# Kernel optimization log

Measured on AMD Instinct MI355X. Metric: run time of the kernel, lower is better.

Reference implementation:

```python
import jax, jax.numpy as jnp
import numpy as np

B, S, E, H = 1, 2048, 1024, 16
D = E // H          # head_dim = 64
SM_SCALE = 0.5      # module default, not 1/sqrt(D)


def setup_inputs() -> dict:
    key = jax.random.key(0)
    ks = jax.random.split(key, 9)
    std = 0.02
    return {
        "x":  jax.random.normal(ks[0], (B, S, E), dtype=jnp.float32),
        "Wq": jax.random.normal(ks[1], (E, E), dtype=jnp.float32) * std,
        "bq": jnp.zeros((E,), dtype=jnp.float32),
        "Wk": jax.random.normal(ks[2], (E, E), dtype=jnp.float32) * std,
        "bk": jnp.zeros((E,), dtype=jnp.float32),
        "Wv": jax.random.normal(ks[3], (E, E), dtype=jnp.float32) * std,
        "bv": jnp.zeros((E,), dtype=jnp.float32),
        "Wo": jax.random.normal(ks[4], (E, E), dtype=jnp.float32) * std,
        "bo": jnp.zeros((E,), dtype=jnp.float32),
    }


def _split_heads(t):
    # [B,S,E] -> [B,H,S,D]
    b, s, _ = t.shape
    return jnp.transpose(t.reshape(b, s, H, D), (0, 2, 1, 3))


def reference(x, Wq, bq, Wk, bk, Wv, bv, Wo, bo):
    # Projections in fp32, then cast to bf16 (matches module's .astype(bf16))
    q = _split_heads((x @ Wq + bq).astype(jnp.bfloat16))
    k = _split_heads((x @ Wk + bk).astype(jnp.bfloat16))
    v = _split_heads((x @ Wv + bv).astype(jnp.bfloat16))

    # Blockwise loop in the original is mathematically full causal attention
    scores = jnp.einsum("bhqd,bhkd->bhqk", q, k) * SM_SCALE  # [B,H,S,S] bf16
    causal = jnp.tril(jnp.ones((S, S), dtype=bool))
    scores = jnp.where(causal[None, None, :, :], scores, -jnp.inf)
    probs = jax.nn.softmax(scores, axis=-1)
    out = jnp.einsum("bhqk,bhkd->bhqd", probs, v)            # [B,H,S,D]

    out = jnp.transpose(out, (0, 2, 1, 3)).reshape(B, S, E)
    # dropout off (is_training=False / rate=0); final projection in fp32
    return out.astype(jnp.float32) @ Wo + bo
```

## Files before the change

### kernel.cpp

```cpp
#include <hip/hip_runtime.h>
#include <hip/hip_bf16.h>

#define S_LEN 2048
#define E_DIM 1024
#define NH    16
#define HD    64
#define SM_SCALE 0.5f

typedef short bf16x8_t __attribute__((ext_vector_type(8)));
typedef float f32x4_t  __attribute__((ext_vector_type(4)));
typedef __bf16 bf16x4_t __attribute__((ext_vector_type(4)));

static __device__ __forceinline__ unsigned short f2bf_bits(float f) {
    return __builtin_bit_cast(unsigned short, (__bf16)f);
}

#define GLD16(gp, lp) __builtin_amdgcn_global_load_lds(                       \
    (const __attribute__((address_space(1))) void*)(gp),                      \
    (__attribute__((address_space(3))) void*)(lp), 16, 0, 0)

__global__ void k_prep(const float* __restrict__ x,
                       const float* __restrict__ Wq, const float* __restrict__ Wk,
                       const float* __restrict__ Wv, const float* __restrict__ Wo,
                       __bf16* __restrict__ xb, __bf16* __restrict__ wt) {
    const int z = blockIdx.z;
    if (z < 4) {
        __shared__ float tile[32][33];
        const float* W = z == 0 ? Wq : z == 1 ? Wk : z == 2 ? Wv : Wo;
        __bf16* o = wt + (size_t)z * E_DIM * E_DIM;
        const int tx = threadIdx.x, ty = threadIdx.y;
        const int bx = blockIdx.x * 32, by = blockIdx.y * 32;
#pragma unroll
        for (int j = 0; j < 32; j += 8)
            tile[ty + j][tx] = W[(size_t)(by + ty + j) * E_DIM + bx + tx];
        __syncthreads();
#pragma unroll
        for (int j = 0; j < 32; j += 8)
            o[(size_t)(bx + ty + j) * E_DIM + by + tx] = (__bf16)tile[tx][ty + j];
    } else {
        const int bid = (z - 4) * 1024 + blockIdx.y * 32 + blockIdx.x;
        const int tid = threadIdx.y * 32 + threadIdx.x;
        const int i = bid * 256 + tid;
        const float4 v = ((const float4*)x)[i];
        bf16x4_t o4;
        o4.x = (__bf16)v.x; o4.y = (__bf16)v.y; o4.z = (__bf16)v.z; o4.w = (__bf16)v.w;
        ((bf16x4_t*)xb)[i] = o4;
    }
}

__global__ __launch_bounds__(256) void k_gemm_qkv(
    const __bf16* __restrict__ xb, const __bf16* __restrict__ wt,
    const float* __restrict__ bq, const float* __restrict__ bk, const float* __restrict__ bv,
    __bf16* __restrict__ qkv) {
    __shared__ __align__(16) unsigned short As[128 * 32];
    __shared__ __align__(16) unsigned short Bs[128 * 32];

    const int z = blockIdx.z;
    const __bf16* Bt = wt + (size_t)z * E_DIM * E_DIM;
    const float* bias = z == 0 ? bq : z == 1 ? bk : bv;
    __bf16* out = qkv + (size_t)z * NH * S_LEN * HD;

    const int tid = threadIdx.x, w = tid >> 6, l = tid & 63;
    const int lm = l & 15, q4 = l >> 4;
    const int bm = blockIdx.y, bn = blockIdx.x;
    const int wm = w >> 1, wn = w & 1;

    const int sm = (w << 4) + (l >> 2);
    const int skk = (l & 3) << 3;
    const __bf16* Ag = xb + (size_t)(bm * 128 + sm) * E_DIM + skk;
    const __bf16* Bg = Bt + (size_t)(bn * 128 + sm) * E_DIM + skk;
    unsigned short* AsW = As + (w << 9);
    unsigned short* BsW = Bs + (w << 9);

    f32x4_t acc[4][4];
#pragma unroll
    for (int i = 0; i < 4; i++)
#pragma unroll
        for (int j = 0; j < 4; j++) { acc[i][j].x = 0.f; acc[i][j].y = 0.f; acc[i][j].z = 0.f; acc[i][j].w = 0.f; }

    for (int k0 = 0; k0 < E_DIM; k0 += 32) {
        __syncthreads();
        GLD16(Ag + k0, AsW);
        GLD16(Ag + (size_t)64 * E_DIM + k0, AsW + 2048);
        GLD16(Bg + k0, BsW);
        GLD16(Bg + (size_t)64 * E_DIM + k0, BsW + 2048);
        __syncthreads();

        bf16x8_t af[4], bfr[4];
#pragma unroll
        for (int mt = 0; mt < 4; mt++)
            af[mt] = *(const bf16x8_t*)&As[(wm * 64 + mt * 16 + lm) * 32 + q4 * 8];
#pragma unroll
        for (int nt = 0; nt < 4; nt++)
            bfr[nt] = *(const bf16x8_t*)&Bs[(wn * 64 + nt * 16 + lm) * 32 + q4 * 8];
#pragma unroll
        for (int mt = 0; mt < 4; mt++)
#pragma unroll
            for (int nt = 0; nt < 4; nt++)
                acc[mt][nt] = __builtin_amdgcn_mfma_f32_16x16x32_bf16(af[mt], bfr[nt], acc[mt][nt], 0, 0, 0);
    }

#pragma unroll
    for (int nt = 0; nt < 4; nt++) {
        const int n = bn * 128 + wn * 64 + nt * 16 + lm;
        const float bval = bias[n];
        const int h = n >> 6, d = n & 63;
        const int tile0 = bm * 2 + wm;
        if (z == 2) {
            const int t4 = d >> 4, flm = d & 15;
#pragma unroll
            for (int mt = 0; mt < 4; mt++) {
                const int q4p = (mt * 2 + (q4 >> 1)) & 3;
                const int j0 = (q4 & 1) * 4;
                __bf16* ob = out + ((((size_t)h * 32 + tile0) * 4 + t4) * 2 + (mt >> 1)) * 512
                                 + (q4p * 16 + flm) * 8 + j0;
                union { unsigned short s[4]; uint2 u; } pk;
#pragma unroll
                for (int i = 0; i < 4; i++) pk.s[i] = f2bf_bits(acc[mt][nt][i] + bval);
                *(uint2*)ob = pk.u;
            }
        } else {
            const float scale = (z == 0) ? SM_SCALE : 1.0f;
            const int c = d >> 5, q4p = (d >> 3) & 3, j = d & 7;
#pragma unroll
            for (int mt = 0; mt < 4; mt++) {
                __bf16* ob = out + ((((size_t)h * 32 + tile0) * 4 + mt) * 2 + c) * 512
                                 + (q4p * 16 + q4 * 4) * 8 + j;
#pragma unroll
                for (int i = 0; i < 4; i++)
                    ob[i * 8] = (__bf16)((acc[mt][nt][i] + bval) * scale);
            }
        }
    }
}

__global__ __launch_bounds__(256, 2) void k_attn(
    const __bf16* __restrict__ Qf, const __bf16* __restrict__ Kf, const __bf16* __restrict__ Vf,
    __bf16* __restrict__ attn) {
    __shared__ __align__(16) unsigned short KVs[2][2][4096];
    __shared__ __align__(16) unsigned short Pl[4][16 * 72];

    const int b = blockIdx.x;
    int qt, h;
    if (b < 256) { qt = 16 + (b >> 4); h = b & 15; }
    else         { qt = 15 - ((b - 256) >> 4); h = (b - 256) & 15; }

    const int tid = threadIdx.x, w = tid >> 6, l = tid & 63;
    const int lm = l & 15, q4 = l >> 4;

    const __bf16* Qb = Qf + ((size_t)h * 32 + qt) * 4096;
    const __bf16* Kb = Kf + (size_t)h * 32 * 4096;
    const __bf16* Vb = Vf + (size_t)h * 32 * 4096;

    bf16x8_t qf[2];
#pragma unroll
    for (int c = 0; c < 2; c++)
        qf[c] = *(const bf16x8_t*)(Qb + ((w * 2 + c) << 9) + l * 8);

    float lacc = 0.f;
    f32x4_t oacc[4];
#pragma unroll
    for (int t = 0; t < 4; t++) { oacc[t].x = 0.f; oacc[t].y = 0.f; oacc[t].z = 0.f; oacc[t].w = 0.f; }

    unsigned short* Pw = Pl[w];

    {
        GLD16(Kb + (w << 9) + l * 8,       &KVs[0][0][(w << 9) + l * 8]);
        GLD16(Kb + ((w + 4) << 9) + l * 8, &KVs[0][0][((w + 4) << 9) + l * 8]);
        GLD16(Vb + (w << 9) + l * 8,       &KVs[0][1][(w << 9) + l * 8]);
        GLD16(Vb + ((w + 4) << 9) + l * 8, &KVs[0][1][((w + 4) << 9) + l * 8]);
    }
    __syncthreads();

    for (int s = 0; s <= qt; s++) {
        const int bb = s & 1;
        if (s < qt) {
            const __bf16* Kg = Kb + (size_t)(s + 1) * 4096;
            const __bf16* Vg = Vb + (size_t)(s + 1) * 4096;
            GLD16(Kg + (w << 9) + l * 8,       &KVs[bb ^ 1][0][(w << 9) + l * 8]);
            GLD16(Kg + ((w + 4) << 9) + l * 8, &KVs[bb ^ 1][0][((w + 4) << 9) + l * 8]);
            GLD16(Vg + (w << 9) + l * 8,       &KVs[bb ^ 1][1][(w << 9) + l * 8]);
            GLD16(Vg + ((w + 4) << 9) + l * 8, &KVs[bb ^ 1][1][((w + 4) << 9) + l * 8]);
        }

        f32x4_t st[4];
#pragma unroll
        for (int t = 0; t < 4; t++) { st[t].x = 0.f; st[t].y = 0.f; st[t].z = 0.f; st[t].w = 0.f; }
#pragma unroll
        for (int t = 0; t < 4; t++) {
            bf16x8_t kf0 = *(const bf16x8_t*)&KVs[bb][0][((t * 2 + 0) << 9) + l * 8];
            bf16x8_t kf1 = *(const bf16x8_t*)&KVs[bb][0][((t * 2 + 1) << 9) + l * 8];
            st[t] = __builtin_amdgcn_mfma_f32_16x16x32_bf16(kf0, qf[0], st[t], 0, 0, 0);
            st[t] = __builtin_amdgcn_mfma_f32_16x16x32_bf16(kf1, qf[1], st[t], 0, 0, 0);
        }
        if (s == qt) {
            const int rowl = w * 16 + lm;
#pragma unroll
            for (int t = 0; t < 4; t++)
#pragma unroll
                for (int i = 0; i < 4; i++) {
                    const int keyl = t * 16 + q4 * 4 + i;
                    st[t][i] = (keyl > rowl) ? 0.f : __expf(st[t][i]);
                }
        } else {
#pragma unroll
            for (int t = 0; t < 4; t++)
#pragma unroll
                for (int i = 0; i < 4; i++) st[t][i] = __expf(st[t][i]);
        }
#pragma unroll
        for (int t = 0; t < 4; t++)
            lacc += (st[t][0] + st[t][1]) + (st[t][2] + st[t][3]);
#pragma unroll
        for (int t = 0; t < 4; t++) {
            union { unsigned short s4[4]; uint2 u; } pk;
#pragma unroll
            for (int i = 0; i < 4; i++) pk.s4[i] = f2bf_bits(st[t][i]);
            *(uint2*)&Pw[lm * 72 + t * 16 + q4 * 4] = pk.u;
        }
#pragma unroll
        for (int c = 0; c < 2; c++) {
            bf16x8_t pf = *(const bf16x8_t*)&Pw[lm * 72 + c * 32 + q4 * 8];
#pragma unroll
            for (int t = 0; t < 4; t++) {
                bf16x8_t vf = *(const bf16x8_t*)&KVs[bb][1][((t * 2 + c) << 9) + l * 8];
                oacc[t] = __builtin_amdgcn_mfma_f32_16x16x32_bf16(vf, pf, oacc[t], 0, 0, 0);
            }
        }
        __syncthreads();
    }

    lacc += __shfl_xor(lacc, 16, 64);
    lacc += __shfl_xor(lacc, 32, 64);
    const float rl = 1.f / lacc;
    const int row = qt * 64 + w * 16 + lm;
#pragma unroll
    for (int t = 0; t < 4; t++) {
        union { unsigned short s4[4]; uint2 u; } pk;
#pragma unroll
        for (int i = 0; i < 4; i++) pk.s4[i] = f2bf_bits(oacc[t][i] * rl);
        *(uint2*)(attn + (size_t)row * E_DIM + h * HD + t * 16 + q4 * 4) = pk.u;
    }
}

__global__ __launch_bounds__(256) void k_gemm_out(
    const __bf16* __restrict__ A, const __bf16* __restrict__ Bt,
    const float* __restrict__ bias, float* __restrict__ out) {
    __shared__ __align__(16) unsigned short As[2][64 * 32];
    __shared__ __align__(16) unsigned short Bs[2][128 * 32];

    const int tid = threadIdx.x, w = tid >> 6, l = tid & 63;
    const int lm = l & 15, q4 = l >> 4;
    const int bm = blockIdx.y, bn = blockIdx.x;
    const int wm = w >> 1, wn = w & 1;

    const int sm = (w << 4) + (l >> 2);
    const int skk = (l & 3) << 3;
    const __bf16* Ag = A + (size_t)(bm * 64 + sm) * E_DIM + skk;
    const __bf16* Bg = Bt + (size_t)(bn * 128 + sm) * E_DIM + skk;
    const int woff = w << 9;

    f32x4_t acc[2][4];
#pragma unroll
    for (int i = 0; i < 2; i++)
#pragma unroll
        for (int j = 0; j < 4; j++) { acc[i][j].x = 0.f; acc[i][j].y = 0.f; acc[i][j].z = 0.f; acc[i][j].w = 0.f; }

    GLD16(Ag, &As[0][woff]);
    GLD16(Bg, &Bs[0][woff]);
    GLD16(Bg + (size_t)64 * E_DIM, &Bs[0][woff + 2048]);
    __syncthreads();

    for (int s = 0; s < 32; s++) {
        const int bb = s & 1;
        if (s < 31) {
            const int k0 = (s + 1) * 32;
            GLD16(Ag + k0, &As[bb ^ 1][woff]);
            GLD16(Bg + k0, &Bs[bb ^ 1][woff]);
            GLD16(Bg + (size_t)64 * E_DIM + k0, &Bs[bb ^ 1][woff + 2048]);
        }

        bf16x8_t af[2], bfr[4];
#pragma unroll
        for (int mt = 0; mt < 2; mt++)
            af[mt] = *(const bf16x8_t*)&As[bb][(wm * 32 + mt * 16 + lm) * 32 + q4 * 8];
#pragma unroll
        for (int nt = 0; nt < 4; nt++)
            bfr[nt] = *(const bf16x8_t*)&Bs[bb][(wn * 64 + nt * 16 + lm) * 32 + q4 * 8];
#pragma unroll
        for (int mt = 0; mt < 2; mt++)
#pragma unroll
            for (int nt = 0; nt < 4; nt++)
                acc[mt][nt] = __builtin_amdgcn_mfma_f32_16x16x32_bf16(af[mt], bfr[nt], acc[mt][nt], 0, 0, 0);
        __syncthreads();
    }

#pragma unroll
    for (int nt = 0; nt < 4; nt++) {
        const int n = bn * 128 + wn * 64 + nt * 16 + lm;
        const float bval = bias[n];
#pragma unroll
        for (int mt = 0; mt < 2; mt++) {
            const int r0 = bm * 64 + wm * 32 + mt * 16 + q4 * 4;
#pragma unroll
            for (int i = 0; i < 4; i++)
                out[(size_t)(r0 + i) * E_DIM + n] = acc[mt][nt][i] + bval;
        }
    }
}

extern "C" void kernel_launch(void* const* d_in, const int* in_sizes, int n_in,
                              void* d_out, int out_size, void* d_ws, size_t ws_size,
                              hipStream_t stream) {
    const float* x  = (const float*)d_in[0];
    const float* Wq = (const float*)d_in[1];
    const float* bq = (const float*)d_in[2];
    const float* Wk = (const float*)d_in[3];
    const float* bk = (const float*)d_in[4];
    const float* Wv = (const float*)d_in[5];
    const float* bv = (const float*)d_in[6];
    const float* Wo = (const float*)d_in[7];
    const float* bo = (const float*)d_in[8];
    float* out = (float*)d_out;

    char* ws = (char*)d_ws;
    __bf16* xb   = (__bf16*)(ws);
    __bf16* wt   = (__bf16*)(ws + ((size_t)4  << 20));
    __bf16* qkv  = (__bf16*)(ws + ((size_t)12 << 20));
    __bf16* attn = (__bf16*)(ws + ((size_t)24 << 20));

    k_prep<<<dim3(32, 32, 6), dim3(32, 8), 0, stream>>>(x, Wq, Wk, Wv, Wo, xb, wt);
    k_gemm_qkv<<<dim3(E_DIM / 128, S_LEN / 128, 3), 256, 0, stream>>>(xb, wt, bq, bk, bv, qkv);
    k_attn<<<dim3(512), 256, 0, stream>>>(
        qkv, qkv + (size_t)NH * S_LEN * HD, qkv + (size_t)2 * NH * S_LEN * HD, attn);
    k_gemm_out<<<dim3(E_DIM / 128, S_LEN / 64), 256, 0, stream>>>(
        attn, wt + (size_t)3 * E_DIM * E_DIM, bo, out);
}
```

Before: 157.4 us.

## Switch attention to 32x32x16 MFMA with split-key waves and LDS reduction

The attention kernel now uses 32x32x16 bf16 MFMA tiles instead of 16x16x32. Each wave covers 32 query rows and half of the 64-key block, and Q/K/V are written in matching fragment layouts by the projection kernel. Waves whose key half lies entirely above the diagonal skip that block. The two key-half partial outputs and row sums are combined through LDS at the end. This aims for higher MFMA throughput and fewer wasted masked tiles, at the cost of a final cross-wave reduction, an extra barrier and higher register pressure from 16-wide accumulators.

```diff
diff --git a/kernel.cpp b/kernel.cpp
--- a/kernel.cpp
+++ b/kernel.cpp
@@ -7,8 +7,9 @@
 #define HD    64
 #define SM_SCALE 0.5f
 
-typedef short bf16x8_t __attribute__((ext_vector_type(8)));
-typedef float f32x4_t  __attribute__((ext_vector_type(4)));
+typedef short bf16x8_t  __attribute__((ext_vector_type(8)));
+typedef float f32x4_t   __attribute__((ext_vector_type(4)));
+typedef float f32x16_t  __attribute__((ext_vector_type(16)));
 typedef __bf16 bf16x4_t __attribute__((ext_vector_type(4)));
 
 static __device__ __forceinline__ unsigned short f2bf_bits(float f) {
@@ -107,25 +108,23 @@
         const int h = n >> 6, d = n & 63;
         const int tile0 = bm * 2 + wm;
         if (z == 2) {
-            const int t4 = d >> 4, flm = d & 15;
+            const int db = d >> 5, dl = d & 31;
 #pragma unroll
             for (int mt = 0; mt < 4; mt++) {
-                const int q4p = (mt * 2 + (q4 >> 1)) & 3;
-                const int j0 = (q4 & 1) * 4;
-                __bf16* ob = out + ((((size_t)h * 32 + tile0) * 4 + t4) * 2 + (mt >> 1)) * 512
-                                 + (q4p * 16 + flm) * 8 + j0;
-                union { unsigned short s[4]; uint2 u; } pk;
-#pragma unroll
-                for (int i = 0; i < 4; i++) pk.s[i] = f2bf_bits(acc[mt][nt][i] + bval);
+                __bf16* ob = out + (((size_t)h * 32 + tile0) * 8 + db * 4 + mt) * 512
+                                 + (dl + (q4 >> 1) * 32) * 8 + (q4 & 1) * 4;
+                union { unsigned short s4[4]; uint2 u; } pk;
+#pragma unroll
+                for (int i = 0; i < 4; i++) pk.s4[i] = f2bf_bits(acc[mt][nt][i] + bval);
                 *(uint2*)ob = pk.u;
             }
         } else {
             const float scale = (z == 0) ? SM_SCALE : 1.0f;
-            const int c = d >> 5, q4p = (d >> 3) & 3, j = d & 7;
+            const int kc = d >> 4, khalf = (d >> 3) & 1, j = d & 7;
 #pragma unroll
             for (int mt = 0; mt < 4; mt++) {
-                __bf16* ob = out + ((((size_t)h * 32 + tile0) * 4 + mt) * 2 + c) * 512
-                                 + (q4p * 16 + q4 * 4) * 8 + j;
+                __bf16* ob = out + (((size_t)h * 32 + tile0) * 8 + (mt >> 1) * 4 + kc) * 512
+                                 + ((mt & 1) * 16 + q4 * 4 + khalf * 32) * 8 + j;
 #pragma unroll
                 for (int i = 0; i < 4; i++)
                     ob[i * 8] = (__bf16)((acc[mt][nt][i] + bval) * scale);
@@ -138,7 +137,7 @@
     const __bf16* __restrict__ Qf, const __bf16* __restrict__ Kf, const __bf16* __restrict__ Vf,
     __bf16* __restrict__ attn) {
     __shared__ __align__(16) unsigned short KVs[2][2][4096];
-    __shared__ __align__(16) unsigned short Pl[4][16 * 72];
+    __shared__ __align__(16) unsigned short Pl[4][32 * 40];
 
     const int b = blockIdx.x;
     int qt, h;
@@ -146,30 +145,31 @@
     else         { qt = 15 - ((b - 256) >> 4); h = (b - 256) & 15; }
 
     const int tid = threadIdx.x, w = tid >> 6, l = tid & 63;
-    const int lm = l & 15, q4 = l >> 4;
+    const int rh = w & 1, kh = w >> 1;
+    const int l31 = l & 31, lh = l >> 5;
 
     const __bf16* Qb = Qf + ((size_t)h * 32 + qt) * 4096;
     const __bf16* Kb = Kf + (size_t)h * 32 * 4096;
     const __bf16* Vb = Vf + (size_t)h * 32 * 4096;
 
-    bf16x8_t qf[2];
-#pragma unroll
-    for (int c = 0; c < 2; c++)
-        qf[c] = *(const bf16x8_t*)(Qb + ((w * 2 + c) << 9) + l * 8);
+    bf16x8_t qf[4];
+#pragma unroll
+    for (int kc = 0; kc < 4; kc++)
+        qf[kc] = *(const bf16x8_t*)(Qb + ((rh * 4 + kc) << 9) + l * 8);
 
     float lacc = 0.f;
-    f32x4_t oacc[4];
-#pragma unroll
-    for (int t = 0; t < 4; t++) { oacc[t].x = 0.f; oacc[t].y = 0.f; oacc[t].z = 0.f; oacc[t].w = 0.f; }
+    f32x16_t oacc[2];
+#pragma unroll
+    for (int db = 0; db < 2; db++)
+#pragma unroll
+        for (int r = 0; r < 16; r++) oacc[db][r] = 0.f;
 
     unsigned short* Pw = Pl[w];
 
-    {
-        GLD16(Kb + (w << 9) + l * 8,       &KVs[0][0][(w << 9) + l * 8]);
-        GLD16(Kb + ((w + 4) << 9) + l * 8, &KVs[0][0][((w + 4) << 9) + l * 8]);
-        GLD16(Vb + (w << 9) + l * 8,       &KVs[0][1][(w << 9) + l * 8]);
-        GLD16(Vb + ((w + 4) << 9) + l * 8, &KVs[0][1][((w + 4) << 9) + l * 8]);
-    }
+    GLD16(Kb + (w << 9) + l * 8,       &KVs[0][0][(w << 9) + l * 8]);
+    GLD16(Kb + ((w + 4) << 9) + l * 8, &KVs[0][0][((w + 4) << 9) + l * 8]);
+    GLD16(Vb + (w << 9) + l * 8,       &KVs[0][1][(w << 9) + l * 8]);
+    GLD16(Vb + ((w + 4) << 9) + l * 8, &KVs[0][1][((w + 4) << 9) + l * 8]);
     __syncthreads();
 
     for (int s = 0; s <= qt; s++) {
@@ -183,63 +183,78 @@
             GLD16(Vg + ((w + 4) << 9) + l * 8, &KVs[bb ^ 1][1][((w + 4) << 9) + l * 8]);
         }
 
-        f32x4_t st[4];
-#pragma unroll
-        for (int t = 0; t < 4; t++) { st[t].x = 0.f; st[t].y = 0.f; st[t].z = 0.f; st[t].w = 0.f; }
-#pragma unroll
-        for (int t = 0; t < 4; t++) {
-            bf16x8_t kf0 = *(const bf16x8_t*)&KVs[bb][0][((t * 2 + 0) << 9) + l * 8];
-            bf16x8_t kf1 = *(const bf16x8_t*)&KVs[bb][0][((t * 2 + 1) << 9) + l * 8];
-            st[t] = __builtin_amdgcn_mfma_f32_16x16x32_bf16(kf0, qf[0], st[t], 0, 0, 0);
-            st[t] = __builtin_amdgcn_mfma_f32_16x16x32_bf16(kf1, qf[1], st[t], 0, 0, 0);
-        }
-        if (s == qt) {
-            const int rowl = w * 16 + lm;
-#pragma unroll
-            for (int t = 0; t < 4; t++)
-#pragma unroll
-                for (int i = 0; i < 4; i++) {
-                    const int keyl = t * 16 + q4 * 4 + i;
-                    st[t][i] = (keyl > rowl) ? 0.f : __expf(st[t][i]);
+        const bool diag = (s == qt);
+        if (!(diag && kh > rh)) {
+            f32x16_t st;
+#pragma unroll
+            for (int r = 0; r < 16; r++) st[r] = 0.f;
+#pragma unroll
+            for (int kc = 0; kc < 4; kc++) {
+                bf16x8_t kf = *(const bf16x8_t*)&KVs[bb][0][((kh * 4 + kc) << 9) + l * 8];
+                st = __builtin_amdgcn_mfma_f32_32x32x16_bf16(kf, qf[kc], st, 0, 0, 0);
+            }
+            if (diag && kh == rh) {
+#pragma unroll
+                for (int r = 0; r < 16; r++) {
+                    const int keyl = (r & 3) + 8 * (r >> 2) + 4 * lh;
+                    st[r] = (keyl > l31) ? 0.f : __expf(st[r]);
                 }
-        } else {
-#pragma unroll
-            for (int t = 0; t < 4; t++)
-#pragma unroll
-                for (int i = 0; i < 4; i++) st[t][i] = __expf(st[t][i]);
-        }
-#pragma unroll
-        for (int t = 0; t < 4; t++)
-            lacc += (st[t][0] + st[t][1]) + (st[t][2] + st[t][3]);
-#pragma unroll
-        for (int t = 0; t < 4; t++) {
-            union { unsigned short s4[4]; uint2 u; } pk;
-#pragma unroll
-            for (int i = 0; i < 4; i++) pk.s4[i] = f2bf_bits(st[t][i]);
-            *(uint2*)&Pw[lm * 72 + t * 16 + q4 * 4] = pk.u;
-        }
-#pragma unroll
-        for (int c = 0; c < 2; c++) {
-            bf16x8_t pf = *(const bf16x8_t*)&Pw[lm * 72 + c * 32 + q4 * 8];
-#pragma unroll
-            for (int t = 0; t < 4; t++) {
-                bf16x8_t vf = *(const bf16x8_t*)&KVs[bb][1][((t * 2 + c) << 9) + l * 8];
-                oacc[t] = __builtin_amdgcn_mfma_f32_16x16x32_bf16(vf, pf, oacc[t], 0, 0, 0);
-            }
-        }
-        __syncthreads();
-    }
-
-    lacc += __shfl_xor(lacc, 16, 64);
-    lacc += __shfl_xor(lacc, 32, 64);
-    const float rl = 1.f / lacc;
-    const int row = qt * 64 + w * 16 + lm;
-#pragma unroll
-    for (int t = 0; t < 4; t++) {
-        union { unsigned short s4[4]; uint2 u; } pk;
-#pragma unroll
-        for (int i = 0; i < 4; i++) pk.s4[i] = f2bf_bits(oacc[t][i] * rl);
-        *(uint2*)(attn + (size_t)row * E_DIM + h * HD + t * 16 + q4 * 4) = pk.u;
+            } else {
+#pragma unroll
+                for (int r = 0; r < 16; r++) st[r] = __expf(st[r]);
+            }
+#pragma unroll
+            for (int r = 0; r < 16; r++) lacc += st[r];
+#pragma unroll
+            for (int a = 0; a < 4; a++) {
+                union { unsigned short s4[4]; uint2 u; } pk;
+#pragma unroll
+                for (int i = 0; i < 4; i++) pk.s4[i] = f2bf_bits(st[a * 4 + i]);
+                *(uint2*)&Pw[l31 * 40 + lh * 4 + a * 8] = pk.u;
+            }
+#pragma unroll
+            for (int c = 0; c < 2; c++) {
+                bf16x8_t pf = *(const bf16x8_t*)&Pw[l31 * 40 + c * 16 + lh * 8];
+#pragma unroll
+                for (int db = 0; db < 2; db++) {
+                    bf16x8_t vf = *(const bf16x8_t*)&KVs[bb][1][((db * 4 + kh * 2 + c) << 9) + l * 8];
+                    oacc[db] = __builtin_amdgcn_mfma_f32_32x32x16_bf16(vf, pf, oacc[db], 0, 0, 0);
+                }
+            }
+        }
+        __syncthreads();
+    }
+
+    __syncthreads();
+    float* Ex = (float*)KVs;
+    if (kh == 1) {
+        float* e = Ex + (rh * 64 + l) * 34;
+#pragma unroll
+        for (int db = 0; db < 2; db++)
+#pragma unroll
+            for (int r = 0; r < 16; r++) e[db * 16 + r] = oacc[db][r];
+        e[32] = lacc;
+    }
+    __syncthreads();
+    if (kh == 0) {
+        const float* e = Ex + (rh * 64 + l) * 34;
+#pragma unroll
+        for (int db = 0; db < 2; db++)
+#pragma unroll
+            for (int r = 0; r < 16; r++) oacc[db][r] += e[db * 16 + r];
+        lacc += e[32];
+        lacc += __shfl_xor(lacc, 32, 64);
+        const float rl = 1.f / lacc;
+        const int row = qt * 64 + rh * 32 + l31;
+#pragma unroll
+        for (int db = 0; db < 2; db++)
+#pragma unroll
+            for (int a = 0; a < 4; a++) {
+                union { unsigned short s4[4]; uint2 u; } pk;
+#pragma unroll
+                for (int i = 0; i < 4; i++) pk.s4[i] = f2bf_bits(oacc[db][a * 4 + i] * rl);
+                *(uint2*)(attn + (size_t)row * E_DIM + h * HD + db * 32 + a * 8 + lh * 4) = pk.u;
+            }
     }
 }
 
```

Result: no change. 154.4 us (median of 2 runs) (-1.9%).
